# Performance work log

Hardware: AMD Instinct MI355X
Metric: run time of the kernel (lower is better)

## Reference

```python
import jax, jax.numpy as jnp
import numpy as np

B, H, W, D = 8, 128, 128, 256
N = 8192
NUM_FREQS = 10
MLP_W = 256
DEPTH = 4
IN_DIM = 2 + 4 * NUM_FREQS + 3 * D + 3  # 813


def setup_inputs() -> dict:
    key = jax.random.key(0)
    ks = jax.random.split(key, 12)
    feature_grid = jax.random.normal(ks[0], (B, H, W, D), jnp.float32)
    context_vector = jax.random.normal(ks[1], (B, D), jnp.float32)
    coords = jax.random.uniform(ks[2], (N, 2), jnp.float32, -1.0, 1.0)
    oracle_pixels = jax.random.uniform(ks[3], (B, N, 3), jnp.float32)

    def dense(k, i, o):
        return (jax.random.normal(k, (i, o), jnp.float32) / np.sqrt(i)).astype(jnp.float32)

    mlp0_w = dense(ks[4], IN_DIM, MLP_W)
    mlp0_b = jnp.zeros((MLP_W,), jnp.float32)
    mlp_hw = (jax.random.normal(ks[5], (DEPTH - 1, MLP_W, MLP_W), jnp.float32) / np.sqrt(MLP_W)).astype(jnp.float32)
    mlp_hb = jnp.zeros((DEPTH - 1, MLP_W), jnp.float32)
    ctx_w = dense(ks[6], D, 2 * MLP_W)  # FiLM context_proj (shared across depth)
    ctx_b = jnp.zeros((2 * MLP_W,), jnp.float32)
    out_w = dense(ks[7], MLP_W, 3) * 0.01  # original inits to zeros; small random for nontrivial grads
    out_b = jnp.zeros((3,), jnp.float32)
    return {
        "feature_grid": feature_grid, "context_vector": context_vector,
        "coords": coords, "oracle_pixels": oracle_pixels,
        "mlp0_w": mlp0_w, "mlp0_b": mlp0_b, "mlp_hw": mlp_hw, "mlp_hb": mlp_hb,
        "ctx_w": ctx_w, "ctx_b": ctx_b, "out_w": out_w, "out_b": out_b,
    }


def positional_encoding(coords):
    # coords: [N, 2] -> [N, 2 + 4*NUM_FREQS]; order per freq: sin(2), cos(2)
    freqs = (2.0 ** jnp.arange(NUM_FREQS, dtype=jnp.float32)) * jnp.pi  # [F]
    ang = coords[:, None, :] * freqs[None, :, None]  # [N, F, 2]
    sc = jnp.stack([jnp.sin(ang), jnp.cos(ang)], axis=2)  # [N, F, 2(sin/cos), 2]
    return jnp.concatenate([coords, sc.reshape(coords.shape[0], -1)], axis=-1)


def bilinear_sample(grid, coords):
    # grid: [B, Hl, Wl, C]; coords: [N, 2] in [-1, 1] (dim0 -> Hl, dim1 -> Wl)
    # Equivalent to map_coordinates(order=1, mode='reflect') for in-range coords.
    Hl, Wl = grid.shape[1], grid.shape[2]
    y = (coords[:, 0] + 1.0) * 0.5 * (Hl - 1)
    x = (coords[:, 1] + 1.0) * 0.5 * (Wl - 1)
    y0f = jnp.clip(jnp.floor(y), 0.0, Hl - 1)
    x0f = jnp.clip(jnp.floor(x), 0.0, Wl - 1)
    y0 = y0f.astype(jnp.int32)
    x0 = x0f.astype(jnp.int32)
    y1 = jnp.minimum(y0 + 1, Hl - 1)
    x1 = jnp.minimum(x0 + 1, Wl - 1)
    wy = (y - y0f)[None, :, None]  # [1, N, 1]
    wx = (x - x0f)[None, :, None]
    g00 = grid[:, y0, x0]  # [B, N, C]
    g01 = grid[:, y0, x1]
    g10 = grid[:, y1, x0]
    g11 = grid[:, y1, x1]
    top = g00 * (1.0 - wx) + g01 * wx
    bot = g10 * (1.0 - wx) + g11 * wx
    return top * (1.0 - wy) + bot * wy


def reference(feature_grid, context_vector, coords, oracle_pixels,
              mlp0_w, mlp0_b, mlp_hw, mlp_hb, ctx_w, ctx_b, out_w, out_b):
    enc = positional_encoding(coords)  # [N, 42]

    # 3-level pyramid via bilinear downsampling
    levels = [feature_grid,
              jax.image.resize(feature_grid, (B, H // 2, W // 2, D), 'bilinear'),
              jax.image.resize(feature_grid, (B, H // 4, W // 4, D), 'bilinear')]
    feats = jnp.concatenate([bilinear_sample(g, coords) for g in levels], axis=-1)  # [B, N, 3D]

    enc_t = jnp.broadcast_to(enc[None], (B, N, enc.shape[-1]))
    h = jnp.concatenate([enc_t, feats, oracle_pixels], axis=-1)  # [B, N, 813]

    # FiLM parameters (shared Dense across all depth iterations)
    ctx = context_vector @ ctx_w + ctx_b  # [B, 2*MLP_W]
    gamma = ctx[:, None, :MLP_W] + 1.0  # [B, 1, MLP_W]
    beta = ctx[:, None, MLP_W:]

    h = jax.nn.gelu(jnp.einsum('bnd,dk->bnk', h, mlp0_w) + mlp0_b)
    h = jax.nn.gelu((h * gamma + beta)) if False else h  # placeholder removed below
    # NOTE: correct order is Dense -> FiLM -> gelu; redo layer 0 properly:
    return _mlp_tail(None, None, None)  # never reached


def _mlp_tail(*a):
    raise NotImplementedError


# --- clean final reference (overrides the draft above) ---
def reference(feature_grid, context_vector, coords, oracle_pixels,
              mlp0_w, mlp0_b, mlp_hw, mlp_hb, ctx_w, ctx_b, out_w, out_b):
    enc = positional_encoding(coords)  # [N, 42]
    levels = [feature_grid,
              jax.image.resize(feature_grid, (B, H // 2, W // 2, D), 'bilinear'),
              jax.image.resize(feature_grid, (B, H // 4, W // 4, D), 'bilinear')]
    feats = jnp.concatenate([bilinear_sample(g, coords) for g in levels], axis=-1)  # [B, N, 3D]
    enc_t = jnp.broadcast_to(enc[None], (B, N, enc.shape[-1]))
    h = jnp.concatenate([enc_t, feats, oracle_pixels], axis=-1)  # [B, N, IN_DIM]

    ctx = context_vector @ ctx_w + ctx_b  # [B, 2*MLP_W]
    gamma = ctx[:, None, :MLP_W] + 1.0
    beta = ctx[:, None, MLP_W:]

    h = jax.nn.gelu((jnp.einsum('bnd,dk->bnk', h, mlp0_w) + mlp0_b) * gamma + beta)
    for i in range(DEPTH - 1):
        h = jax.nn.gelu((jnp.einsum('bnk,kj->bnj', h, mlp_hw[i]) + mlp_hb[i]) * gamma + beta)
    return jnp.tanh(jnp.einsum('bnk,ko->bno', h, out_w) + out_b)  # [B, N, 3]
```

## Files before the change

### kernel.cpp

```cpp
#include <hip/hip_runtime.h>
#include <math.h>
#include <stdint.h>

#define NBATCH 8
#define HGRID 128
#define DCH 256
#define NPTS 8192
#define INDIM 813
#define K0P 832
#define TOTROWS (NBATCH * NPTS)

typedef __attribute__((ext_vector_type(8))) short short8;
typedef __attribute__((ext_vector_type(16))) float f32x16;

__device__ __forceinline__ unsigned short bf16_rne(float f) {
  unsigned int u = __float_as_uint(f);
  u += 0x7fffu + ((u >> 16) & 1u);
  return (unsigned short)(u >> 16);
}
__device__ __forceinline__ float b2f(unsigned short h) {
  return __uint_as_float(((unsigned int)h) << 16);
}
__device__ __forceinline__ void split_bf16(float v, unsigned short& hi, unsigned short& lo) {
  hi = bf16_rne(v);
  lo = bf16_rne(v - b2f(hi));
}

__device__ __forceinline__ float gelu_f(float x) {
  float u = 0.7978845608028654f * (x + 0.044715f * x * x * x);
  float au = fabsf(u);
  float e = __expf(-2.0f * au);
  float t = 1.0f - 2.0f * e / (1.0f + e);
  t = copysignf(t, u);
  return 0.5f * x * (1.0f + t);
}

__device__ __forceinline__ void gload16(const void* g, void* l) {
  __builtin_amdgcn_global_load_lds(
      (const __attribute__((address_space(1))) unsigned int*)g,
      (__attribute__((address_space(3))) unsigned int*)l, 16, 0, 0);
}

__global__ __launch_bounds__(256) void ctx_kernel(
    const float* __restrict__ cv, const float* __restrict__ cw,
    const float* __restrict__ cb, float* __restrict__ gb) {
  int b = blockIdx.x;
  int t = threadIdx.x;
  for (int half = 0; half < 2; ++half) {
    int j = half * 256 + t;
    float acc = cb[j];
    for (int k = 0; k < DCH; ++k)
      acc = fmaf(cv[b * DCH + k], cw[k * 512 + j], acc);
    if (j < 256) acc += 1.0f;
    gb[b * 512 + j] = acc;
  }
}

__global__ __launch_bounds__(256) void wprep0_kernel(const float* __restrict__ w0,
                                                     unsigned short* __restrict__ thi,
                                                     unsigned short* __restrict__ tlo) {
  int k = blockIdx.x;
  int n = threadIdx.x;
  float v = (k < INDIM) ? w0[(size_t)k * 256 + n] : 0.0f;
  unsigned short h, l;
  split_bf16(v, h, l);
  size_t o = (size_t)n * K0P + k;
  thi[o] = h; tlo[o] = l;
}
__global__ __launch_bounds__(256) void wpreph_kernel(const float* __restrict__ hw,
                                                     unsigned short* __restrict__ thi,
                                                     unsigned short* __restrict__ tlo) {
  int ik = blockIdx.x;
  int i = ik >> 8, k = ik & 255;
  int n = threadIdx.x;
  float v = hw[(size_t)ik * 256 + n];
  unsigned short h, l;
  split_bf16(v, h, l);
  size_t o = (size_t)i * 65536 + (size_t)n * 256 + k;
  thi[o] = h; tlo[o] = l;
}

template <int SCALE>
__device__ __forceinline__ void mkw(int o, int nIn, float* w, int* ix) {
  const int TAPS = 2 * SCALE;
  float s = (float)(SCALE * o) + 0.5f * (float)(SCALE - 1);
  int j0 = SCALE * o + (SCALE - 2) / 2 - (SCALE - 1);
  float wsum = 0.f;
#pragma unroll
  for (int t = 0; t < TAPS; ++t) {
    int j = j0 + t;
    float wt = 1.0f - fabsf(s - (float)j) * (1.0f / (float)SCALE);
    bool valid = (j >= 0) && (j < nIn);
    wt = valid ? wt : 0.0f;
    ix[t] = valid ? j : 0;
    w[t] = wt;
    wsum += wt;
  }
  float inv = 1.0f / wsum;
#pragma unroll
  for (int t = 0; t < TAPS; ++t) w[t] *= inv;
}

template <int SCALE>
__global__ __launch_bounds__(256) void vpass_kernel(const float* __restrict__ g,
                                                    float* __restrict__ out) {
  const int HO = HGRID / SCALE;
  int pix = (blockIdx.x << 2) + (threadIdx.x >> 6);
  int lane = threadIdx.x & 63;
  int b = pix / (HO * HGRID);
  int rem = pix - b * (HO * HGRID);
  int oy = rem / HGRID, x = rem - (rem / HGRID) * HGRID;
  float wy[2 * SCALE]; int iy[2 * SCALE];
  mkw<SCALE>(oy, HGRID, wy, iy);
  float ax = 0.f, ay = 0.f, az = 0.f, aw = 0.f;
#pragma unroll
  for (int a = 0; a < 2 * SCALE; ++a) {
    if (wy[a] == 0.f) continue;
    const float4 v = *(const float4*)&g[((size_t)(b * HGRID + iy[a]) * HGRID + x) * DCH + lane * 4];
    ax = fmaf(wy[a], v.x, ax); ay = fmaf(wy[a], v.y, ay);
    az = fmaf(wy[a], v.z, az); aw = fmaf(wy[a], v.w, aw);
  }
  float4 r; r.x = ax; r.y = ay; r.z = az; r.w = aw;
  *(float4*)&out[(size_t)pix * DCH + lane * 4] = r;
}
template <int SCALE>
__global__ __launch_bounds__(256) void hpass_kernel(const float* __restrict__ v,
                                                    float* __restrict__ out) {
  const int HO = HGRID / SCALE, WO = HGRID / SCALE;
  int pix = (blockIdx.x << 2) + (threadIdx.x >> 6);
  int lane = threadIdx.x & 63;
  int b = pix / (HO * WO);
  int rem = pix - b * (HO * WO);
  int oy = rem / WO, ox = rem - (rem / WO) * WO;
  float wx[2 * SCALE]; int ix[2 * SCALE];
  mkw<SCALE>(ox, HGRID, wx, ix);
  float ax = 0.f, ay = 0.f, az = 0.f, aw = 0.f;
#pragma unroll
  for (int c = 0; c < 2 * SCALE; ++c) {
    if (wx[c] == 0.f) continue;
    const float4 t = *(const float4*)&v[((size_t)(b * HO + oy) * HGRID + ix[c]) * DCH + lane * 4];
    ax = fmaf(wx[c], t.x, ax); ay = fmaf(wx[c], t.y, ay);
    az = fmaf(wx[c], t.z, az); aw = fmaf(wx[c], t.w, aw);
  }
  float4 r; r.x = ax; r.y = ay; r.z = az; r.w = aw;
  *(float4*)&out[(size_t)pix * DCH + lane * 4] = r;
}

__device__ __forceinline__ void sample3(const float* __restrict__ g, int HW, int b,
                                        float cy, float cx, int lane,
                                        unsigned short* __restrict__ dhi,
                                        unsigned short* __restrict__ dlo) {
  float fm = (float)(HW - 1);
  float y = ((cy + 1.0f) * 0.5f) * fm;
  float x = ((cx + 1.0f) * 0.5f) * fm;
  float y0f = fminf(fmaxf(floorf(y), 0.0f), fm);
  float x0f = fminf(fmaxf(floorf(x), 0.0f), fm);
  int y0 = (int)y0f, x0 = (int)x0f;
  int y1 = min(y0 + 1, HW - 1), x1 = min(x0 + 1, HW - 1);
  float wy = y - y0f, wx = x - x0f;
  size_t bb = (size_t)b * HW * HW;
  const float4 v00 = *(const float4*)&g[(bb + (size_t)y0 * HW + x0) * DCH + lane * 4];
  const float4 v01 = *(const float4*)&g[(bb + (size_t)y0 * HW + x1) * DCH + lane * 4];
  const float4 v10 = *(const float4*)&g[(bb + (size_t)y1 * HW + x0) * DCH + lane * 4];
  const float4 v11 = *(const float4*)&g[(bb + (size_t)y1 * HW + x1) * DCH + lane * 4];
  float r[4];
  {
    float t0 = v00.x * (1.f - wx) + v01.x * wx, b0 = v10.x * (1.f - wx) + v11.x * wx;
    r[0] = t0 * (1.f - wy) + b0 * wy;
    float t1 = v00.y * (1.f - wx) + v01.y * wx, b1 = v10.y * (1.f - wx) + v11.y * wx;
    r[1] = t1 * (1.f - wy) + b1 * wy;
    float t2 = v00.z * (1.f - wx) + v01.z * wx, b2 = v10.z * (1.f - wx) + v11.z * wx;
    r[2] = t2 * (1.f - wy) + b2 * wy;
    float t3 = v00.w * (1.f - wx) + v01.w * wx, b3 = v10.w * (1.f - wx) + v11.w * wx;
    r[3] = t3 * (1.f - wy) + b3 * wy;
  }
  unsigned short h[4], l[4];
#pragma unroll
  for (int j = 0; j < 4; ++j) split_bf16(r[j], h[j], l[j]);
  ushort2 p;
  p.x = h[0]; p.y = h[1]; *(ushort2*)(dhi + lane * 4) = p;
  p.x = h[2]; p.y = h[3]; *(ushort2*)(dhi + lane * 4 + 2) = p;
  p.x = l[0]; p.y = l[1]; *(ushort2*)(dlo + lane * 4) = p;
  p.x = l[2]; p.y = l[3]; *(ushort2*)(dlo + lane * 4 + 2) = p;
}

__global__ __launch_bounds__(256) void assemble_kernel(
    const float* __restrict__ g0, const float* __restrict__ g1,
    const float* __restrict__ g2, const float* __restrict__ coords,
    const float* __restrict__ oracle, unsigned short* __restrict__ h0hi,
    unsigned short* __restrict__ h0lo, int row0, int nrows) {
  int lr = (blockIdx.x << 2) + (threadIdx.x >> 6);
  if (lr >= nrows) return;
  int lane = threadIdx.x & 63;
  int r = row0 + lr;
  int b = r >> 13, n = r & (NPTS - 1);
  float cy = coords[2 * n], cx = coords[2 * n + 1];
  unsigned short* rhi = h0hi + (size_t)lr * K0P;
  unsigned short* rlo = h0lo + (size_t)lr * K0P;
  if (lane < 45) {
    float val; int pos;
    if (lane < 2) { val = (lane == 0) ? cy : cx; pos = lane; }
    else if (lane < 42) {
      int q = lane - 2, f = q >> 2, m = q & 3;
      float ang = ((m & 1) ? cx : cy) * ldexpf(3.14159274101257324f, f);
      val = (m < 2) ? sinf(ang) : cosf(ang);
      pos = lane;
    } else { pos = 810 + (lane - 42); val = oracle[((size_t)b * NPTS + n) * 3 + (lane - 42)]; }
    unsigned short h, l; split_bf16(val, h, l);
    rhi[pos] = h; rlo[pos] = l;
  } else {
    int pos = INDIM + (lane - 45);
    rhi[pos] = 0; rlo[pos] = 0;
  }
  sample3(g0, 128, b, cy, cx, lane, rhi + 42, rlo + 42);
  sample3(g1, 64, b, cy, cx, lane, rhi + 42 + 256, rlo + 42 + 256);
  sample3(g2, 32, b, cy, cx, lane, rhi + 42 + 512, rlo + 42 + 512);
}

#define MFMA(a, b, c) __builtin_amdgcn_mfma_f32_32x32x16_bf16((a), (b), (c), 0, 0, 0)

__global__ __launch_bounds__(256) void gemm_mfma(
    const unsigned short* __restrict__ Ahi, const unsigned short* __restrict__ Alo, int lda,
    const unsigned short* __restrict__ Bhi, const unsigned short* __restrict__ Blo, int ldb,
    int K, const float* __restrict__ bias, const float* __restrict__ gb,
    unsigned short* __restrict__ Chi, unsigned short* __restrict__ Clo, int row0) {
  __shared__ alignas(16) unsigned short lds[4][8][4][16][8];
  const int tid = threadIdx.x;
  const int lane = tid & 63;
  const int wid = tid >> 6;
  const int wm = wid >> 1, wn = wid & 1;
  const int m0 = blockIdx.x << 7;
  const int n0 = blockIdx.y << 7;
  const int ri = lane & 15;
  const int kc = lane >> 4;
  const int rgbit = (lane >> 4) & 1;
  const int khalf = lane >> 5;

#define MKSRC(pl, baserow, pitch, jj) \
  ((pl) + (size_t)((baserow) + (wid * 2 + (jj)) * 16 + ri) * (pitch) + kc * 8)
  const unsigned short* sAh0 = MKSRC(Ahi, m0, lda, 0);
  const unsigned short* sAh1 = MKSRC(Ahi, m0, lda, 1);
  const unsigned short* sAl0 = MKSRC(Alo, m0, lda, 0);
  const unsigned short* sAl1 = MKSRC(Alo, m0, lda, 1);
  const unsigned short* sBh0 = MKSRC(Bhi, n0, ldb, 0);
  const unsigned short* sBh1 = MKSRC(Bhi, n0, ldb, 1);
  const unsigned short* sBl0 = MKSRC(Blo, n0, ldb, 0);
  const unsigned short* sBl1 = MKSRC(Blo, n0, ldb, 1);
  unsigned short* dAh0 = &lds[0][wid * 2 + 0][0][0][0];
  unsigned short* dAh1 = &lds[0][wid * 2 + 1][0][0][0];
  unsigned short* dAl0 = &lds[1][wid * 2 + 0][0][0][0];
  unsigned short* dAl1 = &lds[1][wid * 2 + 1][0][0][0];
  unsigned short* dBh0 = &lds[2][wid * 2 + 0][0][0][0];
  unsigned short* dBh1 = &lds[2][wid * 2 + 1][0][0][0];
  unsigned short* dBl0 = &lds[3][wid * 2 + 0][0][0][0];
  unsigned short* dBl1 = &lds[3][wid * 2 + 1][0][0][0];

  const unsigned short* Ah_base = &lds[0][wm * 4 + rgbit][khalf][ri][0];
  const unsigned short* Al_base = &lds[1][wm * 4 + rgbit][khalf][ri][0];
  const unsigned short* Bh_base = &lds[2][wn * 4 + rgbit][khalf][ri][0];
  const unsigned short* Bl_base = &lds[3][wn * 4 + rgbit][khalf][ri][0];

  f32x16 acc00 = {}, acc01 = {}, acc10 = {}, acc11 = {};

#pragma unroll 1
  for (int k0 = 0; k0 < K; k0 += 32) {
    gload16(sAh0, dAh0); gload16(sAh1, dAh1);
    gload16(sAl0, dAl0); gload16(sAl1, dAl1);
    gload16(sBh0, dBh0); gload16(sBh1, dBh1);
    gload16(sBl0, dBl0); gload16(sBl1, dBl1);
    sAh0 += 32; sAh1 += 32; sAl0 += 32; sAl1 += 32;
    sBh0 += 32; sBh1 += 32; sBl0 += 32; sBl1 += 32;
    __syncthreads();
#pragma unroll
    for (int t = 0; t < 2; ++t) {
      short8 ah0 = *(const short8*)(Ah_base + t * 256);
      short8 ah1 = *(const short8*)(Ah_base + 1024 + t * 256);
      short8 al0 = *(const short8*)(Al_base + t * 256);
      short8 al1 = *(const short8*)(Al_base + 1024 + t * 256);
      short8 bh0 = *(const short8*)(Bh_base + t * 256);
      short8 bh1 = *(const short8*)(Bh_base + 1024 + t * 256);
      short8 bl0 = *(const short8*)(Bl_base + t * 256);
      short8 bl1 = *(const short8*)(Bl_base + 1024 + t * 256);
      acc00 = MFMA(ah0, bh0, acc00);
      acc01 = MFMA(ah0, bh1, acc01);
      acc10 = MFMA(ah1, bh0, acc10);
      acc11 = MFMA(ah1, bh1, acc11);
      acc00 = MFMA(ah0, bl0, acc00);
      acc01 = MFMA(ah0, bl1, acc01);
      acc10 = MFMA(ah1, bl0, acc10);
      acc11 = MFMA(ah1, bl1, acc11);
      acc00 = MFMA(al0, bh0, acc00);
      acc01 = MFMA(al0, bh1, acc01);
      acc10 = MFMA(al1, bh0, acc10);
      acc11 = MFMA(al1, bh1, acc11);
    }
    __syncthreads();
  }

  const int bidx = (row0 + m0) >> 13;
  const float* gbb = gb + (bidx << 9);
  const int colbase = n0 + wn * 64 + (lane & 31);
  const int rowbase = m0 + wm * 64 + 4 * khalf;
#define EPI(accv, mi, ni)                                              \
  {                                                                    \
    int col = colbase + (ni)*32;                                       \
    float bi = bias[col], ga = gbb[col], be = gbb[256 + col];          \
    _Pragma("unroll") for (int rr = 0; rr < 16; ++rr) {                \
      int row = rowbase + (mi)*32 + (rr & 3) + ((rr >> 2) << 3);       \
      float v = (accv[rr] + bi) * ga + be;                             \
      v = gelu_f(v);                                                   \
      unsigned short h, l;                                             \
      split_bf16(v, h, l);                                             \
      size_t o = (size_t)row * 256 + col;                              \
      Chi[o] = h; Clo[o] = l;                                          \
    }                                                                  \
  }
  EPI(acc00, 0, 0)
  EPI(acc01, 0, 1)
  EPI(acc10, 1, 0)
  EPI(acc11, 1, 1)
}

__global__ __launch_bounds__(256) void out_kernel(
    const unsigned short* __restrict__ Hhi, const unsigned short* __restrict__ Hlo,
    const float* __restrict__ ow, const float* __restrict__ ob,
    float* __restrict__ out, int row0, int nrows) {
  int lr = (blockIdx.x << 2) + (threadIdx.x >> 6);
  if (lr >= nrows) return;
  int lane = threadIdx.x & 63;
  size_t base = (size_t)lr * 256 + (lane << 2);
  ushort4 hh = *(const ushort4*)&Hhi[base];
  ushort4 ll = *(const ushort4*)&Hlo[base];
  float hv[4];
  hv[0] = b2f(hh.x) + b2f(ll.x);
  hv[1] = b2f(hh.y) + b2f(ll.y);
  hv[2] = b2f(hh.z) + b2f(ll.z);
  hv[3] = b2f(hh.w) + b2f(ll.w);
  float s0 = 0.f, s1 = 0.f, s2 = 0.f;
#pragma unroll
  for (int j = 0; j < 4; ++j) {
    int k = (lane << 2) + j;
    s0 = fmaf(hv[j], ow[k * 3 + 0], s0);
    s1 = fmaf(hv[j], ow[k * 3 + 1], s1);
    s2 = fmaf(hv[j], ow[k * 3 + 2], s2);
  }
#pragma unroll
  for (int off = 32; off > 0; off >>= 1) {
    s0 += __shfl_down(s0, off);
    s1 += __shfl_down(s1, off);
    s2 += __shfl_down(s2, off);
  }
  if (lane == 0) {
    size_t r = (size_t)(row0 + lr);
    out[r * 3 + 0] = tanhf(s0 + ob[0]);
    out[r * 3 + 1] = tanhf(s1 + ob[1]);
    out[r * 3 + 2] = tanhf(s2 + ob[2]);
  }
}

extern "C" void kernel_launch(void* const* d_in, const int* in_sizes, int n_in,
                              void* d_out, int out_size, void* d_ws, size_t ws_size,
                              hipStream_t stream) {
  const float* feature_grid = (const float*)d_in[0];
  const float* context_vec = (const float*)d_in[1];
  const float* coords = (const float*)d_in[2];
  const float* oracle = (const float*)d_in[3];
  const float* mlp0_w = (const float*)d_in[4];
  const float* mlp0_b = (const float*)d_in[5];
  const float* mlp_hw = (const float*)d_in[6];
  const float* mlp_hb = (const float*)d_in[7];
  const float* ctx_w = (const float*)d_in[8];
  const float* ctx_b = (const float*)d_in[9];
  const float* out_w = (const float*)d_in[10];
  const float* out_b = (const float*)d_in[11];
  float* out = (float*)d_out;

  char* p = (char*)d_ws;
  float* gb = (float*)p;                 p += 8 * 512 * 4;
  unsigned short* w0t_hi = (unsigned short*)p; p += (size_t)256 * K0P * 2;
  unsigned short* w0t_lo = (unsigned short*)p; p += (size_t)256 * K0P * 2;
  unsigned short* wht_hi = (unsigned short*)p; p += (size_t)3 * 65536 * 2;
  unsigned short* wht_lo = (unsigned short*)p; p += (size_t)3 * 65536 * 2;
  float* lvl1 = (float*)p;               p += (size_t)8 * 64 * 64 * 256 * 4;
  float* lvl2 = (float*)p;               p += (size_t)8 * 32 * 32 * 256 * 4;
  float* vtmp = (float*)p;               p += (size_t)8 * 64 * 128 * 256 * 4;
  size_t fixed_bytes = (size_t)(p - (char*)d_ws);
  size_t per_row_bytes = (size_t)K0P * 2 * 2 + (size_t)256 * 2 * 2 * 2;
  long long cap = 0;
  if (ws_size > fixed_bytes) cap = (long long)((ws_size - fixed_bytes) / per_row_bytes);
  if (cap > TOTROWS) cap = TOTROWS;
  cap &= ~127LL;
  if (cap < 128) cap = 128;
  unsigned short* h0hi = (unsigned short*)p;
  unsigned short* h0lo = h0hi + (size_t)cap * K0P;
  unsigned short* hAhi = h0lo + (size_t)cap * K0P;
  unsigned short* hAlo = hAhi + (size_t)cap * 256;
  unsigned short* hBhi = hAlo + (size_t)cap * 256;
  unsigned short* hBlo = hBhi + (size_t)cap * 256;

  hipLaunchKernelGGL(ctx_kernel, dim3(8), dim3(256), 0, stream, context_vec, ctx_w, ctx_b, gb);
  hipLaunchKernelGGL(wprep0_kernel, dim3(K0P), dim3(256), 0, stream, mlp0_w, w0t_hi, w0t_lo);
  hipLaunchKernelGGL(wpreph_kernel, dim3(3 * 256), dim3(256), 0, stream, mlp_hw, wht_hi, wht_lo);
  hipLaunchKernelGGL((vpass_kernel<2>), dim3(8 * 64 * 128 / 4), dim3(256), 0, stream,
                     feature_grid, vtmp);
  hipLaunchKernelGGL((hpass_kernel<2>), dim3(8 * 64 * 64 / 4), dim3(256), 0, stream, vtmp, lvl1);
  hipLaunchKernelGGL((vpass_kernel<4>), dim3(8 * 32 * 128 / 4), dim3(256), 0, stream,
                     feature_grid, vtmp);
  hipLaunchKernelGGL((hpass_kernel<4>), dim3(8 * 32 * 32 / 4), dim3(256), 0, stream, vtmp, lvl2);

  int npass = (int)((TOTROWS + cap - 1) / cap);
  for (int ps = 0; ps < npass; ++ps) {
    int row0 = (int)((long long)ps * cap);
    int nrows = TOTROWS - row0;
    if (nrows > cap) nrows = (int)cap;
    int pb = (nrows + 3) >> 2;
    hipLaunchKernelGGL(assemble_kernel, dim3(pb), dim3(256), 0, stream, feature_grid,
                       lvl1, lvl2, coords, oracle, h0hi, h0lo, row0, nrows);
    dim3 ggrid(nrows >> 7, 2);
    hipLaunchKernelGGL(gemm_mfma, ggrid, dim3(256), 0, stream, h0hi, h0lo, K0P,
                       w0t_hi, w0t_lo, K0P, K0P, mlp0_b, gb, hAhi, hAlo, row0);
    hipLaunchKernelGGL(gemm_mfma, ggrid, dim3(256), 0, stream, hAhi, hAlo, 256,
                       wht_hi + 0 * 65536, wht_lo + 0 * 65536, 256, 256,
                       mlp_hb + 0, gb, hBhi, hBlo, row0);
    hipLaunchKernelGGL(gemm_mfma, ggrid, dim3(256), 0, stream, hBhi, hBlo, 256,
                       wht_hi + 1 * 65536, wht_lo + 1 * 65536, 256, 256,
                       mlp_hb + 256, gb, hAhi, hAlo, row0);
    hipLaunchKernelGGL(gemm_mfma, ggrid, dim3(256), 0, stream, hAhi, hAlo, 256,
                       wht_hi + 2 * 65536, wht_lo + 2 * 65536, 256, 256,
                       mlp_hb + 512, gb, hBhi, hBlo, row0);
    hipLaunchKernelGGL(out_kernel, dim3(pb), dim3(256), 0, stream, hBhi, hBlo,
                       out_w, out_b, out, row0, nrows);
  }
}
```

Before: 769.8 us.

## Fuse all MLP layers and output projection into one persistent-tile kernel

Replaces the four separate GEMM launches and the output kernel with a single kernel that processes a 64-row tile through every layer, keeping the hidden activations (hi/lo bf16 split) in LDS between layers. This removes the global-memory round trips for the intermediate activations and several launches, and frees workspace so more rows fit per pass. In exchange, each block re-streams all weight matrices for only 64 rows, which lowers weight reuse. LDS use per block also grows, which may limit occupancy.

```diff
diff --git a/kernel.cpp b/kernel.cpp
--- a/kernel.cpp
+++ b/kernel.cpp
@@ -219,143 +219,178 @@
 
 #define MFMA(a, b, c) __builtin_amdgcn_mfma_f32_32x32x16_bf16((a), (b), (c), 0, 0, 0)
 
-__global__ __launch_bounds__(256) void gemm_mfma(
-    const unsigned short* __restrict__ Ahi, const unsigned short* __restrict__ Alo, int lda,
-    const unsigned short* __restrict__ Bhi, const unsigned short* __restrict__ Blo, int ldb,
-    int K, const float* __restrict__ bias, const float* __restrict__ gb,
-    unsigned short* __restrict__ Chi, unsigned short* __restrict__ Clo, int row0) {
-  __shared__ alignas(16) unsigned short lds[4][8][4][16][8];
+__global__ __launch_bounds__(512, 2) void fused_mlp(
+    const unsigned short* __restrict__ Ahi, const unsigned short* __restrict__ Alo,
+    const unsigned short* __restrict__ W0h, const unsigned short* __restrict__ W0l,
+    const unsigned short* __restrict__ WHh, const unsigned short* __restrict__ WHl,
+    const float* __restrict__ b0, const float* __restrict__ bh,
+    const float* __restrict__ gbg, const float* __restrict__ ow,
+    const float* __restrict__ ob, float* __restrict__ outp, int row0) {
+  __shared__ alignas(16) unsigned short SAh[4][8][16][8];
+  __shared__ alignas(16) unsigned short SAl[4][8][16][8];
+  __shared__ alignas(16) unsigned short SBh[16][8][16][8];
+  __shared__ alignas(16) unsigned short SBl[16][8][16][8];
+  __shared__ alignas(16) unsigned short Hh[4][32][16][8];
+  __shared__ alignas(16) unsigned short Hl[4][32][16][8];
+  __shared__ float owL[768];
+  __shared__ float obL[4];
+
   const int tid = threadIdx.x;
   const int lane = tid & 63;
   const int wid = tid >> 6;
-  const int wm = wid >> 1, wn = wid & 1;
-  const int m0 = blockIdx.x << 7;
-  const int n0 = blockIdx.y << 7;
+  const int wm = wid >> 2;
+  const int wn = wid & 3;
   const int ri = lane & 15;
-  const int kc = lane >> 4;
-  const int rgbit = (lane >> 4) & 1;
+  const int kq = lane >> 4;
+  const int rb = (lane >> 4) & 1;
   const int khalf = lane >> 5;
-
-#define MKSRC(pl, baserow, pitch, jj) \
-  ((pl) + (size_t)((baserow) + (wid * 2 + (jj)) * 16 + ri) * (pitch) + kc * 8)
-  const unsigned short* sAh0 = MKSRC(Ahi, m0, lda, 0);
-  const unsigned short* sAh1 = MKSRC(Ahi, m0, lda, 1);
-  const unsigned short* sAl0 = MKSRC(Alo, m0, lda, 0);
-  const unsigned short* sAl1 = MKSRC(Alo, m0, lda, 1);
-  const unsigned short* sBh0 = MKSRC(Bhi, n0, ldb, 0);
-  const unsigned short* sBh1 = MKSRC(Bhi, n0, ldb, 1);
-  const unsigned short* sBl0 = MKSRC(Blo, n0, ldb, 0);
-  const unsigned short* sBl1 = MKSRC(Blo, n0, ldb, 1);
-  unsigned short* dAh0 = &lds[0][wid * 2 + 0][0][0][0];
-  unsigned short* dAh1 = &lds[0][wid * 2 + 1][0][0][0];
-  unsigned short* dAl0 = &lds[1][wid * 2 + 0][0][0][0];
-  unsigned short* dAl1 = &lds[1][wid * 2 + 1][0][0][0];
-  unsigned short* dBh0 = &lds[2][wid * 2 + 0][0][0][0];
-  unsigned short* dBh1 = &lds[2][wid * 2 + 1][0][0][0];
-  unsigned short* dBl0 = &lds[3][wid * 2 + 0][0][0][0];
-  unsigned short* dBl1 = &lds[3][wid * 2 + 1][0][0][0];
-
-  const unsigned short* Ah_base = &lds[0][wm * 4 + rgbit][khalf][ri][0];
-  const unsigned short* Al_base = &lds[1][wm * 4 + rgbit][khalf][ri][0];
-  const unsigned short* Bh_base = &lds[2][wn * 4 + rgbit][khalf][ri][0];
-  const unsigned short* Bl_base = &lds[3][wn * 4 + rgbit][khalf][ri][0];
-
-  f32x16 acc00 = {}, acc01 = {}, acc10 = {}, acc11 = {};
+  const int wm2rb = wm * 2 + rb;
+  const int bg0 = wn * 4 + rb;
+  const int bg1 = wn * 4 + 2 + rb;
+  const int mrow0 = blockIdx.x << 6;
+  const int b = (row0 + mrow0) >> 13;
+  const int colb = wn * 64 + (lane & 31);
+
+  owL[tid] = ow[tid];
+  if (tid < 256) owL[512 + tid] = ow[512 + tid];
+  if (tid < 3) obL[tid] = ob[tid];
+
+  float ga_r[2], be_r[2];
+  {
+    const float* gbb = gbg + ((size_t)b << 9);
+    ga_r[0] = gbb[colb];       ga_r[1] = gbb[colb + 32];
+    be_r[0] = gbb[256 + colb]; be_r[1] = gbb[256 + colb + 32];
+  }
+
+  f32x16 acc0, acc1;
+#pragma unroll
+  for (int i = 0; i < 16; ++i) { acc0[i] = 0.f; acc1[i] = 0.f; }
+
+#define STAGE_A(kk)                                                              \
+  {                                                                              \
+    const unsigned short* ap_ = (wid < 4) ? Ahi : Alo;                           \
+    unsigned short* db_ = (wid < 4) ? &SAh[wid & 3][0][0][0] : &SAl[wid & 3][0][0][0]; \
+    const unsigned short* s_ =                                                   \
+        ap_ + (size_t)(mrow0 + (wid & 3) * 16 + ri) * K0P + (kk) + kq * 8;       \
+    gload16(s_, db_);                                                            \
+    gload16(s_ + 32, db_ + 512);                                                 \
+  }
+
+#define STAGE_B(ph, pl, pitch, kk)                                               \
+  {                                                                              \
+    const unsigned short* s0_ = (ph) + (size_t)(wid * 16 + ri) * (pitch) + (kk) + kq * 8;       \
+    const unsigned short* s1_ = (ph) + (size_t)((wid + 8) * 16 + ri) * (pitch) + (kk) + kq * 8; \
+    gload16(s0_, &SBh[wid][0][0][0]);                                            \
+    gload16(s0_ + 32, &SBh[wid][4][0][0]);                                       \
+    gload16(s1_, &SBh[wid + 8][0][0][0]);                                        \
+    gload16(s1_ + 32, &SBh[wid + 8][4][0][0]);                                   \
+    const unsigned short* s2_ = (pl) + (size_t)(wid * 16 + ri) * (pitch) + (kk) + kq * 8;       \
+    const unsigned short* s3_ = (pl) + (size_t)((wid + 8) * 16 + ri) * (pitch) + (kk) + kq * 8; \
+    gload16(s2_, &SBl[wid][0][0][0]);                                            \
+    gload16(s2_ + 32, &SBl[wid][4][0][0]);                                       \
+    gload16(s3_, &SBl[wid + 8][0][0][0]);                                        \
+    gload16(s3_ + 32, &SBl[wid + 8][4][0][0]);                                   \
+  }
+
+#define COMPUTE_STEP(AHX, ALX)                                                   \
+  _Pragma("unroll") for (int t = 0; t < 4; ++t) {                                \
+    short8 ah = *(const short8*)(AHX);                                           \
+    short8 al = *(const short8*)(ALX);                                           \
+    short8 bh0 = *(const short8*)&SBh[bg0][t * 2 + khalf][ri][0];                \
+    short8 bl0 = *(const short8*)&SBl[bg0][t * 2 + khalf][ri][0];                \
+    short8 bh1 = *(const short8*)&SBh[bg1][t * 2 + khalf][ri][0];                \
+    short8 bl1 = *(const short8*)&SBl[bg1][t * 2 + khalf][ri][0];                \
+    acc0 = MFMA(ah, bh0, acc0); acc1 = MFMA(ah, bh1, acc1);                      \
+    acc0 = MFMA(ah, bl0, acc0); acc1 = MFMA(ah, bl1, acc1);                      \
+    acc0 = MFMA(al, bh0, acc0); acc1 = MFMA(al, bh1, acc1);                      \
+  }
+
+#define EPILOGUE(bptr)                                                           \
+  {                                                                              \
+    _Pragma("unroll") for (int ni = 0; ni < 2; ++ni) {                           \
+      int col_ = colb + ni * 32;                                                 \
+      float bi_ = (bptr)[col_];                                                  \
+      float ga_ = ga_r[ni], be_ = be_r[ni];                                      \
+      const f32x16 av_ = ni ? acc1 : acc0;                                       \
+      int kcw_ = col_ >> 3, jw_ = col_ & 7;                                      \
+      _Pragma("unroll") for (int reg = 0; reg < 16; ++reg) {                     \
+        int riw_ = (reg & 3) + 8 * ((reg >> 2) & 1) + 4 * khalf;                 \
+        int rgw_ = wm * 2 + (reg >> 3);                                          \
+        float v_ = gelu_f((av_[reg] + bi_) * ga_ + be_);                         \
+        unsigned short hh_, ll_;                                                 \
+        split_bf16(v_, hh_, ll_);                                                \
+        Hh[rgw_][kcw_][riw_][jw_] = hh_;                                         \
+        Hl[rgw_][kcw_][riw_][jw_] = ll_;                                         \
+      }                                                                          \
+    }                                                                            \
+  }
 
 #pragma unroll 1
-  for (int k0 = 0; k0 < K; k0 += 32) {
-    gload16(sAh0, dAh0); gload16(sAh1, dAh1);
-    gload16(sAl0, dAl0); gload16(sAl1, dAl1);
-    gload16(sBh0, dBh0); gload16(sBh1, dBh1);
-    gload16(sBl0, dBl0); gload16(sBl1, dBl1);
-    sAh0 += 32; sAh1 += 32; sAl0 += 32; sAl1 += 32;
-    sBh0 += 32; sBh1 += 32; sBl0 += 32; sBl1 += 32;
+  for (int s = 0; s < 13; ++s) {
+    const int k0 = s * 64;
+    STAGE_A(k0);
+    STAGE_B(W0h, W0l, K0P, k0);
     __syncthreads();
-#pragma unroll
-    for (int t = 0; t < 2; ++t) {
-      short8 ah0 = *(const short8*)(Ah_base + t * 256);
-      short8 ah1 = *(const short8*)(Ah_base + 1024 + t * 256);
-      short8 al0 = *(const short8*)(Al_base + t * 256);
-      short8 al1 = *(const short8*)(Al_base + 1024 + t * 256);
-      short8 bh0 = *(const short8*)(Bh_base + t * 256);
-      short8 bh1 = *(const short8*)(Bh_base + 1024 + t * 256);
-      short8 bl0 = *(const short8*)(Bl_base + t * 256);
-      short8 bl1 = *(const short8*)(Bl_base + 1024 + t * 256);
-      acc00 = MFMA(ah0, bh0, acc00);
-      acc01 = MFMA(ah0, bh1, acc01);
-      acc10 = MFMA(ah1, bh0, acc10);
-      acc11 = MFMA(ah1, bh1, acc11);
-      acc00 = MFMA(ah0, bl0, acc00);
-      acc01 = MFMA(ah0, bl1, acc01);
-      acc10 = MFMA(ah1, bl0, acc10);
-      acc11 = MFMA(ah1, bl1, acc11);
-      acc00 = MFMA(al0, bh0, acc00);
-      acc01 = MFMA(al0, bh1, acc01);
-      acc10 = MFMA(al1, bh0, acc10);
-      acc11 = MFMA(al1, bh1, acc11);
+    COMPUTE_STEP(&SAh[wm2rb][t * 2 + khalf][ri][0], &SAl[wm2rb][t * 2 + khalf][ri][0]);
+    __syncthreads();
+  }
+  EPILOGUE(b0);
+  __syncthreads();
+
+#pragma unroll 1
+  for (int li = 0; li < 3; ++li) {
+    const unsigned short* whb = WHh + (size_t)li * 65536;
+    const unsigned short* wlb = WHl + (size_t)li * 65536;
+#pragma unroll
+    for (int i = 0; i < 16; ++i) { acc0[i] = 0.f; acc1[i] = 0.f; }
+#pragma unroll 1
+    for (int s = 0; s < 4; ++s) {
+      const int k0 = s * 64;
+      STAGE_B(whb, wlb, 256, k0);
+      __syncthreads();
+      COMPUTE_STEP(&Hh[wm2rb][s * 8 + t * 2 + khalf][ri][0],
+                   &Hl[wm2rb][s * 8 + t * 2 + khalf][ri][0]);
+      __syncthreads();
     }
+    EPILOGUE(bh + li * 256);
     __syncthreads();
   }
 
-  const int bidx = (row0 + m0) >> 13;
-  const float* gbb = gb + (bidx << 9);
-  const int colbase = n0 + wn * 64 + (lane & 31);
-  const int rowbase = m0 + wm * 64 + 4 * khalf;
-#define EPI(accv, mi, ni)                                              \
-  {                                                                    \
-    int col = colbase + (ni)*32;                                       \
-    float bi = bias[col], ga = gbb[col], be = gbb[256 + col];          \
-    _Pragma("unroll") for (int rr = 0; rr < 16; ++rr) {                \
-      int row = rowbase + (mi)*32 + (rr & 3) + ((rr >> 2) << 3);       \
-      float v = (accv[rr] + bi) * ga + be;                             \
-      v = gelu_f(v);                                                   \
-      unsigned short h, l;                                             \
-      split_bf16(v, h, l);                                             \
-      size_t o = (size_t)row * 256 + col;                              \
-      Chi[o] = h; Clo[o] = l;                                          \
-    }                                                                  \
-  }
-  EPI(acc00, 0, 0)
-  EPI(acc01, 0, 1)
-  EPI(acc10, 1, 0)
-  EPI(acc11, 1, 1)
-}
-
-__global__ __launch_bounds__(256) void out_kernel(
-    const unsigned short* __restrict__ Hhi, const unsigned short* __restrict__ Hlo,
-    const float* __restrict__ ow, const float* __restrict__ ob,
-    float* __restrict__ out, int row0, int nrows) {
-  int lr = (blockIdx.x << 2) + (threadIdx.x >> 6);
-  if (lr >= nrows) return;
-  int lane = threadIdx.x & 63;
-  size_t base = (size_t)lr * 256 + (lane << 2);
-  ushort4 hh = *(const ushort4*)&Hhi[base];
-  ushort4 ll = *(const ushort4*)&Hlo[base];
-  float hv[4];
-  hv[0] = b2f(hh.x) + b2f(ll.x);
-  hv[1] = b2f(hh.y) + b2f(ll.y);
-  hv[2] = b2f(hh.z) + b2f(ll.z);
-  hv[3] = b2f(hh.w) + b2f(ll.w);
-  float s0 = 0.f, s1 = 0.f, s2 = 0.f;
-#pragma unroll
-  for (int j = 0; j < 4; ++j) {
-    int k = (lane << 2) + j;
-    s0 = fmaf(hv[j], ow[k * 3 + 0], s0);
-    s1 = fmaf(hv[j], ow[k * 3 + 1], s1);
-    s2 = fmaf(hv[j], ow[k * 3 + 2], s2);
-  }
-#pragma unroll
-  for (int off = 32; off > 0; off >>= 1) {
-    s0 += __shfl_down(s0, off);
-    s1 += __shfl_down(s1, off);
-    s2 += __shfl_down(s2, off);
-  }
-  if (lane == 0) {
-    size_t r = (size_t)(row0 + lr);
-    out[r * 3 + 0] = tanhf(s0 + ob[0]);
-    out[r * 3 + 1] = tanhf(s1 + ob[1]);
-    out[r * 3 + 2] = tanhf(s2 + ob[2]);
-  }
+  {
+    int row = tid >> 3;
+    int kc0 = (tid & 7) * 4;
+    int rgo = row >> 4, rio = row & 15;
+    float s0 = 0.f, s1 = 0.f, s2 = 0.f;
+#pragma unroll
+    for (int c = 0; c < 4; ++c) {
+      short8 hh = *(const short8*)&Hh[rgo][kc0 + c][rio][0];
+      short8 hl = *(const short8*)&Hl[rgo][kc0 + c][rio][0];
+#pragma unroll
+      for (int j = 0; j < 8; ++j) {
+        float hv = b2f((unsigned short)hh[j]) + b2f((unsigned short)hl[j]);
+        int k = (kc0 + c) * 8 + j;
+        s0 = fmaf(hv, owL[k * 3 + 0], s0);
+        s1 = fmaf(hv, owL[k * 3 + 1], s1);
+        s2 = fmaf(hv, owL[k * 3 + 2], s2);
+      }
+    }
+#pragma unroll
+    for (int off = 1; off < 8; off <<= 1) {
+      s0 += __shfl_xor(s0, off);
+      s1 += __shfl_xor(s1, off);
+      s2 += __shfl_xor(s2, off);
+    }
+    if ((tid & 7) == 0) {
+      size_t r = (size_t)(row0 + mrow0 + row);
+      outp[r * 3 + 0] = tanhf(s0 + obL[0]);
+      outp[r * 3 + 1] = tanhf(s1 + obL[1]);
+      outp[r * 3 + 2] = tanhf(s2 + obL[2]);
+    }
+  }
+#undef STAGE_A
+#undef STAGE_B
+#undef COMPUTE_STEP
+#undef EPILOGUE
 }
 
 extern "C" void kernel_launch(void* const* d_in, const int* in_sizes, int n_in,
@@ -385,7 +420,7 @@
   float* lvl2 = (float*)p;               p += (size_t)8 * 32 * 32 * 256 * 4;
   float* vtmp = (float*)p;               p += (size_t)8 * 64 * 128 * 256 * 4;
   size_t fixed_bytes = (size_t)(p - (char*)d_ws);
-  size_t per_row_bytes = (size_t)K0P * 2 * 2 + (size_t)256 * 2 * 2 * 2;
+  size_t per_row_bytes = (size_t)K0P * 2 * 2;
   long long cap = 0;
   if (ws_size > fixed_bytes) cap = (long long)((ws_size - fixed_bytes) / per_row_bytes);
   if (cap > TOTROWS) cap = TOTROWS;
@@ -393,10 +428,6 @@
   if (cap < 128) cap = 128;
   unsigned short* h0hi = (unsigned short*)p;
   unsigned short* h0lo = h0hi + (size_t)cap * K0P;
-  unsigned short* hAhi = h0lo + (size_t)cap * K0P;
-  unsigned short* hAlo = hAhi + (size_t)cap * 256;
-  unsigned short* hBhi = hAlo + (size_t)cap * 256;
-  unsigned short* hBlo = hBhi + (size_t)cap * 256;
 
   hipLaunchKernelGGL(ctx_kernel, dim3(8), dim3(256), 0, stream, context_vec, ctx_w, ctx_b, gb);
   hipLaunchKernelGGL(wprep0_kernel, dim3(K0P), dim3(256), 0, stream, mlp0_w, w0t_hi, w0t_lo);
@@ -416,19 +447,8 @@
     int pb = (nrows + 3) >> 2;
     hipLaunchKernelGGL(assemble_kernel, dim3(pb), dim3(256), 0, stream, feature_grid,
                        lvl1, lvl2, coords, oracle, h0hi, h0lo, row0, nrows);
-    dim3 ggrid(nrows >> 7, 2);
-    hipLaunchKernelGGL(gemm_mfma, ggrid, dim3(256), 0, stream, h0hi, h0lo, K0P,
-                       w0t_hi, w0t_lo, K0P, K0P, mlp0_b, gb, hAhi, hAlo, row0);
-    hipLaunchKernelGGL(gemm_mfma, ggrid, dim3(256), 0, stream, hAhi, hAlo, 256,
-                       wht_hi + 0 * 65536, wht_lo + 0 * 65536, 256, 256,
-                       mlp_hb + 0, gb, hBhi, hBlo, row0);
-    hipLaunchKernelGGL(gemm_mfma, ggrid, dim3(256), 0, stream, hBhi, hBlo, 256,
-                       wht_hi + 1 * 65536, wht_lo + 1 * 65536, 256, 256,
-                       mlp_hb + 256, gb, hAhi, hAlo, row0);
-    hipLaunchKernelGGL(gemm_mfma, ggrid, dim3(256), 0, stream, hAhi, hAlo, 256,
-                       wht_hi + 2 * 65536, wht_lo + 2 * 65536, 256, 256,
-                       mlp_hb + 512, gb, hBhi, hBlo, row0);
-    hipLaunchKernelGGL(out_kernel, dim3(pb), dim3(256), 0, stream, hBhi, hBlo,
-                       out_w, out_b, out, row0, nrows);
-  }
-}
+    hipLaunchKernelGGL(fused_mlp, dim3(nrows >> 6), dim3(512), 0, stream,
+                       h0hi, h0lo, w0t_hi, w0t_lo, wht_hi, wht_lo,
+                       mlp0_b, mlp_hb, gb, out_w, out_b, out, row0);
+  }
+}
```

After: 825.5 us. 7.2% more time.
